# Kernel optimization log

Measured on AMD Instinct MI355X. Metric: run time of the kernel, lower is better.

## Reference

```python
import jax, jax.numpy as jnp
from jax import lax
import numpy as np

N_NODES = 100000
N_EDGES = 524288
W_MUL = np.float32((2 ** 0.5) * (5 ** -0.5))  # he_std * lrmul, use_wscale=True
TWO_PI = np.float32(2 * np.pi)


def setup_inputs() -> dict:
    key = jax.random.key(0)
    k1, k2, k3, k4, k5 = jax.random.split(key, 5)
    edges = jax.random.randint(k1, (N_EDGES, 2), 0, N_NODES, dtype=jnp.int64)
    nodes_feature = jax.random.normal(k2, (N_NODES, 2), dtype=jnp.float32)
    # nn.init.uniform_(empty(5), 0, 2*pi) * init_std with init_std = 1.0
    weight = jax.random.uniform(k3, (5,), dtype=jnp.float32) * TWO_PI
    lin_w = jax.random.normal(k4, (2, 16), dtype=jnp.float32) * (1.0 / np.sqrt(16.0))
    lin_b = jax.random.normal(k5, (2,), dtype=jnp.float32) * 0.1
    return {"edges": edges, "nodes_feature": nodes_feature, "weight": weight,
            "lin_w": lin_w, "lin_b": lin_b}


def _circuit_unitary(weight):
    # per-qubit u = Rz(w2) @ Ry(w1) @ Rx(w0); same gates on both qubits -> U = kron(u, u)
    w = weight * W_MUL
    h = w / 2.0
    c, s = jnp.cos(h), jnp.sin(h)
    rx = jnp.stack([jnp.stack([c[0] + 0j, -1j * s[0]]),
                    jnp.stack([-1j * s[0], c[0] + 0j])]).astype(jnp.complex64)
    ry = jnp.stack([jnp.stack([c[1] + 0j, -s[1] + 0j]),
                    jnp.stack([s[1] + 0j, c[1] + 0j])]).astype(jnp.complex64)
    ez = jnp.exp(-1j * h[2].astype(jnp.complex64))
    rz = jnp.stack([jnp.stack([ez, 0 * ez]),
                    jnp.stack([0 * ez, jnp.conj(ez)])]).astype(jnp.complex64)
    u = rz @ ry @ rx
    return jnp.kron(u, u)  # [4,4] complex64


def reference(edges, nodes_feature, weight, lin_w, lin_b):
    U = _circuit_unitary(weight)
    # per-edge amplitude-encoding density matrix rho = c c^T / ||c||^2
    f = jnp.concatenate([nodes_feature[edges[:, 0]],
                         nodes_feature[edges[:, 1]]], axis=1)  # [E,4]
    rho = (f[:, :, None] * f[:, None, :]) / jnp.sum(f * f, axis=1)[:, None, None]
    rho = rho.astype(jnp.complex64)  # [E,4,4]
    # M_i = U rho_i U^dag, batched
    M = jnp.einsum('ab,ebc,dc->ead', U, rho, jnp.conj(U))  # [E,4,4]
    # sequential left-to-right chain product over edges
    def step(carry, m):
        return carry @ m, None
    chain, _ = lax.scan(step, jnp.eye(4, dtype=jnp.complex64), M)
    # .view(1,16).float() in torch: flatten then take real part
    x = jnp.real(chain).reshape(1, 16).astype(jnp.float32)
    logits = x @ lin_w.T + lin_b
    return jax.nn.softmax(logits, axis=1)
```

## Files before the change

kernel.cpp:

```cpp
#include <hip/hip_runtime.h>
#include <math.h>


#define W_MUL 0.63245553203367586640f
#define LN2   0.69314718055994530942
#define TPB   256

struct C { float re, im; };
__device__ __forceinline__ C cmul(C a, C b) {
    return { a.re * b.re - a.im * b.im, a.re * b.im + a.im * b.re };
}
__device__ __forceinline__ C cadd(C a, C b) { return { a.re + b.re, a.im + b.im }; }

__device__ __forceinline__ void build_U(const float* __restrict__ w, C U[4][4]) {
    float h0 = w[0] * W_MUL * 0.5f, h1 = w[1] * W_MUL * 0.5f, h2 = w[2] * W_MUL * 0.5f;
    float c0 = cosf(h0), s0 = sinf(h0);
    float c1 = cosf(h1), s1 = sinf(h1);
    float c2 = cosf(h2), s2 = sinf(h2);
    C rx[2][2] = { { {c0, 0.f}, {0.f, -s0} }, { {0.f, -s0}, {c0, 0.f} } };
    C ry[2][2] = { { {c1, 0.f}, {-s1, 0.f} }, { {s1, 0.f}, {c1, 0.f} } };
    C rz[2][2] = { { {c2, -s2}, {0.f, 0.f} }, { {0.f, 0.f}, {c2, s2} } };
    C t[2][2], u[2][2];
    for (int i = 0; i < 2; i++)
        for (int j = 0; j < 2; j++) {
            C a = {0.f, 0.f};
            for (int k = 0; k < 2; k++) a = cadd(a, cmul(ry[i][k], rx[k][j]));
            t[i][j] = a;
        }
    for (int i = 0; i < 2; i++)
        for (int j = 0; j < 2; j++) {
            C a = {0.f, 0.f};
            for (int k = 0; k < 2; k++) a = cadd(a, cmul(rz[i][k], t[k][j]));
            u[i][j] = a;
        }
    for (int a = 0; a < 2; a++)
        for (int b = 0; b < 2; b++)
            for (int c = 0; c < 2; c++)
                for (int d = 0; d < 2; d++)
                    U[2 * a + c][2 * b + d] = cmul(u[a][b], u[c][d]);
}

__device__ __forceinline__ void edge_v2(float2 fa, float2 fb, const C U[4][4], C v[4]) {
    float f[4] = { fa.x, fa.y, fb.x, fb.y };
    float n2 = f[0] * f[0] + f[1] * f[1] + f[2] * f[2] + f[3] * f[3];
    float inv = rsqrtf(n2);
    #pragma unroll
    for (int k = 0; k < 4; k++) {
        float re = 0.f, im = 0.f;
        #pragma unroll
        for (int j = 0; j < 4; j++) {
            re += U[k][j].re * f[j];
            im += U[k][j].im * f[j];
        }
        v[k] = { re * inv, im * inv };
    }
}

__global__ void __launch_bounds__(TPB)
k_part(const int* __restrict__ edges, const float2* __restrict__ nf,
       int nitems, int E, double* __restrict__ pL, int* __restrict__ pC) {
    int t = blockIdx.x * TPB + threadIdx.x;
    int i0 = 2 * t;
    int lane = threadIdx.x & 63;
    int Em1 = E - 1;

    double lsum = 0.0;
    int neg = 0;

    if (i0 < nitems + 1 && i0 <= Em1 - 1) {
        int4 er = *(const int4*)(edges + 4 * t);
        float2 fa0 = nf[er.x], fb0 = nf[er.y];
        float2 fa1 = nf[er.z], fb1 = nf[er.w];
        float n0 = fa0.x * fa0.x + fa0.y * fa0.y + fb0.x * fb0.x + fb0.y * fb0.y;
        float n1 = fa1.x * fa1.x + fa1.y * fa1.y + fb1.x * fb1.x + fb1.y * fb1.y;

        float2 fa2, fb2;
        float n2v;
        fa2.x = __shfl_down(fa0.x, 1, 64);
        fa2.y = __shfl_down(fa0.y, 1, 64);
        fb2.x = __shfl_down(fb0.x, 1, 64);
        fb2.y = __shfl_down(fb0.y, 1, 64);
        n2v   = __shfl_down(n0, 1, 64);
        if (lane == 63) {
            int r2 = (i0 + 2 <= Em1) ? (i0 + 2) : Em1;
            int2 e2 = *(const int2*)(edges + 2 * r2);
            fa2 = nf[e2.x];
            fb2 = nf[e2.y];
            n2v = fa2.x * fa2.x + fa2.y * fa2.y + fb2.x * fb2.x + fb2.y * fb2.y;
        }

        double num = 1.0, den = 1.0;
        if (i0 < nitems) {
            float d0 = fa0.x * fa1.x + fa0.y * fa1.y + fb0.x * fb1.x + fb0.y * fb1.y;
            num *= (double)(d0 * d0);
            den *= (double)(n0 * n1);
            neg += (d0 < 0.f) ? 1 : 0;
        }
        if (i0 + 1 < nitems) {
            float d1 = fa1.x * fa2.x + fa1.y * fa2.y + fb1.x * fb2.x + fb1.y * fb2.y;
            num *= (double)(d1 * d1);
            den *= (double)(n1 * n2v);
            neg += (d1 < 0.f) ? 1 : 0;
        }
        double Rt = num / den;
        int ex;
        double mf = frexp(Rt, &ex);
        lsum = 0.5 * ((double)ex * LN2 + (double)logf((float)mf));
    }

    for (int off = 32; off; off >>= 1) {
        lsum += __shfl_down(lsum, off, 64);
        neg  += __shfl_down(neg, off, 64);
    }
    __shared__ double sl[TPB / 64];
    __shared__ int    sn[TPB / 64];
    int wid = threadIdx.x >> 6;
    if (lane == 0) { sl[wid] = lsum; sn[wid] = neg; }
    __syncthreads();
    if (threadIdx.x == 0) {
        double L = lsum; int N = neg;
        for (int w = 1; w < TPB / 64; w++) { L += sl[w]; N += sn[w]; }
        pL[blockIdx.x] = L;
        pC[blockIdx.x] = N;
    }
}

__global__ void __launch_bounds__(TPB)
k_fin(const int* __restrict__ edges, const float2* __restrict__ nf,
      const float* __restrict__ weight, const float* __restrict__ lin_w,
      const float* __restrict__ lin_b, int E, int nparts,
      const double* __restrict__ pL, const int* __restrict__ pC,
      float* __restrict__ out) {
    int t = threadIdx.x;
    double L = 0.0; int N = 0;
    for (int i = t; i < nparts; i += TPB) { L += pL[i]; N += pC[i]; }
    for (int off = 32; off; off >>= 1) {
        L += __shfl_down(L, off, 64);
        N += __shfl_down(N, off, 64);
    }
    __shared__ double sl2[TPB / 64];
    __shared__ int    sn2[TPB / 64];
    int wid = t >> 6, lane = t & 63;
    if (lane == 0) { sl2[wid] = L; sn2[wid] = N; }
    __syncthreads();
    if (t != 0) return;
    for (int w = 1; w < TPB / 64; w++) { L += sl2[w]; N += sn2[w]; }

    C U[4][4];
    build_U(weight, U);
    C v0[4], vl[4];
    edge_v2(nf[edges[0]], nf[edges[1]], U, v0);
    edge_v2(nf[edges[2 * (E - 1)]], nf[edges[2 * (E - 1) + 1]], U, vl);

    float s_re;
    if (!(L > -85.0)) s_re = 0.f;
    else              s_re = (float)((N & 1) ? -exp(L) : exp(L));

    float x[16];
    for (int a = 0; a < 4; a++)
        for (int d = 0; d < 4; d++)
            x[4 * a + d] = s_re * (v0[a].re * vl[d].re + v0[a].im * vl[d].im);

    float l0 = lin_b[0], l1 = lin_b[1];
    for (int k = 0; k < 16; k++) {
        l0 += x[k] * lin_w[k];
        l1 += x[k] * lin_w[16 + k];
    }
    float mx = fmaxf(l0, l1);
    float e0 = expf(l0 - mx), e1 = expf(l1 - mx);
    float inv = 1.f / (e0 + e1);
    out[0] = e0 * inv;
    out[1] = e1 * inv;
}

extern "C" void kernel_launch(void* const* d_in, const int* in_sizes, int n_in,
                              void* d_out, int out_size, void* d_ws, size_t ws_size,
                              hipStream_t stream) {
    const int*    edges  = (const int*)d_in[0];
    const float2* nf     = (const float2*)d_in[1];
    const float*  weight = (const float*)d_in[2];
    const float*  lin_w  = (const float*)d_in[3];
    const float*  lin_b  = (const float*)d_in[4];
    float* out = (float*)d_out;

    int E = in_sizes[0] / 2;
    int nitems = E - 1;

    int per_block = TPB * 2;
    int blocks = (nitems + per_block - 1) / per_block;

    double* pL = (double*)d_ws;
    int*    pC = (int*)(pL + blocks);

    k_part<<<blocks, TPB, 0, stream>>>(edges, nf, nitems, E, pL, pC);
    k_fin<<<1, TPB, 0, stream>>>(edges, nf, weight, lin_w, lin_b,
                                 E, blocks, pL, pC, out);
}
```

Baseline: 15.77 us.

## Fuse partial and final reduction kernels via last-block atomic counter

```diff
diff --git a/kernel.cpp b/kernel.cpp
--- a/kernel.cpp
+++ b/kernel.cpp
@@ -5,6 +5,8 @@
 #define W_MUL 0.63245553203367586640f
 #define LN2   0.69314718055994530942
 #define TPB   256
+#define GRP   32
+#define CSTR  16
 
 struct C { float re, im; };
 __device__ __forceinline__ C cmul(C a, C b) {
@@ -57,8 +59,12 @@
 }
 
 __global__ void __launch_bounds__(TPB)
-k_part(const int* __restrict__ edges, const float2* __restrict__ nf,
-       int nitems, int E, double* __restrict__ pL, int* __restrict__ pC) {
+k_all(const int* __restrict__ edges, const float2* __restrict__ nf,
+      const float* __restrict__ weight, const float* __restrict__ lin_w,
+      const float* __restrict__ lin_b, int nitems, int E,
+      int nblocks, int ngroups,
+      int* __restrict__ ctr, double* __restrict__ pL, int* __restrict__ pC,
+      float* __restrict__ out) {
     int t = blockIdx.x * TPB + threadIdx.x;
     int i0 = 2 * t;
     int lane = threadIdx.x & 63;
@@ -67,7 +73,7 @@
     double lsum = 0.0;
     int neg = 0;
 
-    if (i0 < nitems + 1 && i0 <= Em1 - 1) {
+    if (i0 <= Em1 - 1) {
         int4 er = *(const int4*)(edges + 4 * t);
         float2 fa0 = nf[er.x], fb0 = nf[er.y];
         float2 fa1 = nf[er.z], fb1 = nf[er.w];
@@ -114,43 +120,53 @@
     }
     __shared__ double sl[TPB / 64];
     __shared__ int    sn[TPB / 64];
+    __shared__ int    amLast;
     int wid = threadIdx.x >> 6;
     if (lane == 0) { sl[wid] = lsum; sn[wid] = neg; }
     __syncthreads();
+
     if (threadIdx.x == 0) {
         double L = lsum; int N = neg;
         for (int w = 1; w < TPB / 64; w++) { L += sl[w]; N += sn[w]; }
-        pL[blockIdx.x] = L;
-        pC[blockIdx.x] = N;
-    }
-}
-
-__global__ void __launch_bounds__(TPB)
-k_fin(const int* __restrict__ edges, const float2* __restrict__ nf,
-      const float* __restrict__ weight, const float* __restrict__ lin_w,
-      const float* __restrict__ lin_b, int E, int nparts,
-      const double* __restrict__ pL, const int* __restrict__ pC,
-      float* __restrict__ out) {
-    int t = threadIdx.x;
+        __hip_atomic_store(&pL[blockIdx.x], L, __ATOMIC_RELAXED, __HIP_MEMORY_SCOPE_AGENT);
+        __hip_atomic_store(&pC[blockIdx.x], N, __ATOMIC_RELAXED, __HIP_MEMORY_SCOPE_AGENT);
+        __threadfence();
+        amLast = 0;
+        int g = blockIdx.x / GRP;
+        int gsize = min(GRP, nblocks - g * GRP);
+        int old = __hip_atomic_fetch_add(&ctr[g * CSTR], 1,
+                                         __ATOMIC_ACQ_REL, __HIP_MEMORY_SCOPE_AGENT);
+        if (old == gsize - 1) {
+            int old2 = __hip_atomic_fetch_add(&ctr[ngroups * CSTR], 1,
+                                              __ATOMIC_ACQ_REL, __HIP_MEMORY_SCOPE_AGENT);
+            if (old2 == ngroups - 1) amLast = 1;
+        }
+    }
+    __syncthreads();
+    if (!amLast) return;
+
+    __threadfence();
     double L = 0.0; int N = 0;
-    for (int i = t; i < nparts; i += TPB) { L += pL[i]; N += pC[i]; }
+    for (int i = threadIdx.x; i < nblocks; i += TPB) {
+        L += __hip_atomic_load(&pL[i], __ATOMIC_RELAXED, __HIP_MEMORY_SCOPE_AGENT);
+        N += __hip_atomic_load(&pC[i], __ATOMIC_RELAXED, __HIP_MEMORY_SCOPE_AGENT);
+    }
     for (int off = 32; off; off >>= 1) {
         L += __shfl_down(L, off, 64);
         N += __shfl_down(N, off, 64);
     }
     __shared__ double sl2[TPB / 64];
     __shared__ int    sn2[TPB / 64];
-    int wid = t >> 6, lane = t & 63;
     if (lane == 0) { sl2[wid] = L; sn2[wid] = N; }
     __syncthreads();
-    if (t != 0) return;
+    if (threadIdx.x != 0) return;
     for (int w = 1; w < TPB / 64; w++) { L += sl2[w]; N += sn2[w]; }
 
     C U[4][4];
     build_U(weight, U);
     C v0[4], vl[4];
     edge_v2(nf[edges[0]], nf[edges[1]], U, v0);
-    edge_v2(nf[edges[2 * (E - 1)]], nf[edges[2 * (E - 1) + 1]], U, vl);
+    edge_v2(nf[edges[2 * Em1]], nf[edges[2 * Em1 + 1]], U, vl);
 
     float s_re;
     if (!(L > -85.0)) s_re = 0.f;
@@ -188,11 +204,15 @@
 
     int per_block = TPB * 2;
     int blocks = (nitems + per_block - 1) / per_block;
-
-    double* pL = (double*)d_ws;
-    int*    pC = (int*)(pL + blocks);
-
-    k_part<<<blocks, TPB, 0, stream>>>(edges, nf, nitems, E, pL, pC);
-    k_fin<<<1, TPB, 0, stream>>>(edges, nf, weight, lin_w, lin_b,
-                                 E, blocks, pL, pC, out);
-}
+    int ngroups = (blocks + GRP - 1) / GRP;
+
+    int*    ctr = (int*)d_ws;
+    double* pL  = (double*)((char*)d_ws + 4096);
+    int*    pC  = (int*)(pL + blocks);
+
+    hipMemsetAsync(ctr, 0, (size_t)(ngroups + 1) * CSTR * sizeof(int), stream);
+
+    k_all<<<blocks, TPB, 0, stream>>>(edges, nf, weight, lin_w, lin_b,
+                                      nitems, E, blocks, ngroups,
+                                      ctr, pL, pC, out);
+}
```

Measured after the change: 49.96 us. 3.17x slower.

## Fuse partial and final reduction into one kernel with slotted atomics

Applied to the files above, without the earlier changes.

```diff
diff --git a/kernel.cpp b/kernel.cpp
--- a/kernel.cpp
+++ b/kernel.cpp
@@ -5,6 +5,9 @@
 #define W_MUL 0.63245553203367586640f
 #define LN2   0.69314718055994530942
 #define TPB   256
+#define NSLOT 32
+#define DSTR  8
+#define ISTR  16
 
 struct C { float re, im; };
 __device__ __forceinline__ C cmul(C a, C b) {
@@ -57,8 +60,12 @@
 }
 
 __global__ void __launch_bounds__(TPB)
-k_part(const int* __restrict__ edges, const float2* __restrict__ nf,
-       int nitems, int E, double* __restrict__ pL, int* __restrict__ pC) {
+k_all(const int* __restrict__ edges, const float2* __restrict__ nf,
+      const float* __restrict__ weight, const float* __restrict__ lin_w,
+      const float* __restrict__ lin_b, int nitems, int E, int nblocks,
+      double* __restrict__ pL, int* __restrict__ pC,
+      int* __restrict__ ctr, int* __restrict__ gctr,
+      float* __restrict__ out) {
     int t = blockIdx.x * TPB + threadIdx.x;
     int i0 = 2 * t;
     int lane = threadIdx.x & 63;
@@ -67,7 +74,7 @@
     double lsum = 0.0;
     int neg = 0;
 
-    if (i0 < nitems + 1 && i0 <= Em1 - 1) {
+    if (i0 <= Em1 - 1) {
         int4 er = *(const int4*)(edges + 4 * t);
         float2 fa0 = nf[er.x], fb0 = nf[er.y];
         float2 fa1 = nf[er.z], fb1 = nf[er.w];
@@ -117,44 +124,44 @@
     int wid = threadIdx.x >> 6;
     if (lane == 0) { sl[wid] = lsum; sn[wid] = neg; }
     __syncthreads();
-    if (threadIdx.x == 0) {
-        double L = lsum; int N = neg;
-        for (int w = 1; w < TPB / 64; w++) { L += sl[w]; N += sn[w]; }
-        pL[blockIdx.x] = L;
-        pC[blockIdx.x] = N;
-    }
-}
-
-__global__ void __launch_bounds__(TPB)
-k_fin(const int* __restrict__ edges, const float2* __restrict__ nf,
-      const float* __restrict__ weight, const float* __restrict__ lin_w,
-      const float* __restrict__ lin_b, int E, int nparts,
-      const double* __restrict__ pL, const int* __restrict__ pC,
-      float* __restrict__ out) {
-    int t = threadIdx.x;
-    double L = 0.0; int N = 0;
-    for (int i = t; i < nparts; i += TPB) { L += pL[i]; N += pC[i]; }
-    for (int off = 32; off; off >>= 1) {
-        L += __shfl_down(L, off, 64);
-        N += __shfl_down(N, off, 64);
-    }
-    __shared__ double sl2[TPB / 64];
-    __shared__ int    sn2[TPB / 64];
-    int wid = t >> 6, lane = t & 63;
-    if (lane == 0) { sl2[wid] = L; sn2[wid] = N; }
-    __syncthreads();
-    if (t != 0) return;
-    for (int w = 1; w < TPB / 64; w++) { L += sl2[w]; N += sn2[w]; }
+    if (threadIdx.x != 0) return;
+
+    double L = lsum; int N = neg;
+    for (int w = 1; w < TPB / 64; w++) { L += sl[w]; N += sn[w]; }
+
+    int s = blockIdx.x & (NSLOT - 1);
+    __hip_atomic_fetch_add(&pL[s * DSTR], L, __ATOMIC_RELAXED, __HIP_MEMORY_SCOPE_AGENT);
+    __hip_atomic_fetch_add(&pC[s * ISTR], N, __ATOMIC_RELAXED, __HIP_MEMORY_SCOPE_AGENT);
+    asm volatile("s_waitcnt vmcnt(0)" ::: "memory");
+
+    int expected = (nblocks - s + NSLOT - 1) >> 5;
+    int old = __hip_atomic_fetch_add(&ctr[s * ISTR], 1,
+                                     __ATOMIC_RELAXED, __HIP_MEMORY_SCOPE_AGENT);
+    if (old != expected - 1) return;
+
+    int nres = (nblocks < NSLOT) ? nblocks : NSLOT;
+    int old2 = __hip_atomic_fetch_add(gctr, 1,
+                                      __ATOMIC_RELAXED, __HIP_MEMORY_SCOPE_AGENT);
+    if (old2 != nres - 1) return;
+
+    __threadfence();
+    double Lt = 0.0; int Nt = 0;
+    #pragma unroll
+    for (int i = 0; i < NSLOT; i++) {
+        if (i >= nres) break;
+        Lt += __hip_atomic_load(&pL[i * DSTR], __ATOMIC_RELAXED, __HIP_MEMORY_SCOPE_AGENT);
+        Nt += __hip_atomic_load(&pC[i * ISTR], __ATOMIC_RELAXED, __HIP_MEMORY_SCOPE_AGENT);
+    }
 
     C U[4][4];
     build_U(weight, U);
     C v0[4], vl[4];
     edge_v2(nf[edges[0]], nf[edges[1]], U, v0);
-    edge_v2(nf[edges[2 * (E - 1)]], nf[edges[2 * (E - 1) + 1]], U, vl);
+    edge_v2(nf[edges[2 * Em1]], nf[edges[2 * Em1 + 1]], U, vl);
 
     float s_re;
-    if (!(L > -85.0)) s_re = 0.f;
-    else              s_re = (float)((N & 1) ? -exp(L) : exp(L));
+    if (!(Lt > -85.0)) s_re = 0.f;
+    else               s_re = (float)((Nt & 1) ? -exp(Lt) : exp(Lt));
 
     float x[16];
     for (int a = 0; a < 4; a++)
@@ -189,10 +196,14 @@
     int per_block = TPB * 2;
     int blocks = (nitems + per_block - 1) / per_block;
 
-    double* pL = (double*)d_ws;
-    int*    pC = (int*)(pL + blocks);
-
-    k_part<<<blocks, TPB, 0, stream>>>(edges, nf, nitems, E, pL, pC);
-    k_fin<<<1, TPB, 0, stream>>>(edges, nf, weight, lin_w, lin_b,
-                                 E, blocks, pL, pC, out);
-}
+    double* pL   = (double*)d_ws;
+    int*    pC   = (int*)((char*)d_ws + 2048);
+    int*    ctr  = (int*)((char*)d_ws + 4096);
+    int*    gctr = (int*)((char*)d_ws + 6144);
+
+    hipMemsetAsync(d_ws, 0, 8192, stream);
+
+    k_all<<<blocks, TPB, 0, stream>>>(edges, nf, weight, lin_w, lin_b,
+                                      nitems, E, blocks,
+                                      pL, pC, ctr, gctr, out);
+}
```

After: 21.15 us. +34.1%, slower.
